# Kernel optimization log

Measured on AMD Instinct MI355X. Metric: run time of the kernel, lower is better.

Reference implementation:

```python
import jax, jax.numpy as jnp
import numpy as np

B, S, H, L, O = 128, 2048, 128, 2, 2  # batch, seq, hidden(=input), layers, output


def setup_inputs() -> dict:
    key = jax.random.key(0)
    k1, k2, k3, k4, k5 = jax.random.split(key, 5)
    std = 1.0 / np.sqrt(H)
    x_data = jax.random.normal(k1, (B, S, H), dtype=jnp.float32)
    x_length = jax.random.randint(k2, (B,), 0, S, dtype=jnp.int32)
    x_label = jax.random.uniform(k3, (B,), dtype=jnp.float32)
    # torch Linear layout: y = x @ W.T ; init uniform(-1/sqrt(H), 1/sqrt(H))
    Wx2h = jax.random.uniform(k4, (L, 2 * H, H), minval=-std, maxval=std, dtype=jnp.float32)
    Wfc = jax.random.uniform(k5, (L, O, H), minval=-std, maxval=std, dtype=jnp.float32)
    return {"x_data": x_data, "x_length": x_length, "x_label": x_label,
            "Wx2h": Wx2h, "Wfc": Wfc}


def reference(x_data, x_length, x_label, Wx2h, Wfc):
    Bn, Sn, Hn = x_data.shape
    Ln = Wx2h.shape[0]
    # valid-timestep mask: seq index < x_length[i]
    mask = (jnp.arange(Sn)[None, :] < x_length[:, None]).astype(x_data.dtype)  # [B,S]

    def step(carry, inp):
        S1, S2 = carry            # each [L,B,H]
        x_t, m_t = inp            # [B,H], [B]
        h = x_t
        out = None
        S1_new, S2_new = [], []
        for l in range(Ln):
            gate = h @ Wx2h[l].T                    # [B,2H]
            m1, m2 = jnp.split(gate, 2, axis=1)
            s1n = S1[l] + jnp.tanh(m1)
            s2n = S2[l] + jnp.tanh(m2)
            Fu = jax.nn.relu(s1n)
            h = (1.0 - Fu) * s2n + Fu * S2[l]       # hy
            out = jax.nn.softmax(h @ Wfc[l].T, axis=1)  # [B,O]
            S1_new.append(s1n)
            S2_new.append(s2n)
        loss_t = m_t * (x_label - jax.nn.sigmoid(out[:, 1])) ** 2  # [B]
        return (jnp.stack(S1_new), jnp.stack(S2_new)), loss_t

    S0 = jnp.zeros((Ln, Bn, Hn), x_data.dtype)
    xs = (jnp.swapaxes(x_data, 0, 1), mask.T)  # time-major [S,B,H], [S,B]
    _, losses = jax.lax.scan(step, (S0, S0), xs)
    return jnp.sum(losses)
```

## Files before the change

### kernel.cpp

```cpp
#include <hip/hip_runtime.h>

typedef __bf16 bf16;
typedef __bf16 bf16x8 __attribute__((ext_vector_type(8)));
typedef float floatx4 __attribute__((ext_vector_type(4)));

#define BATCH 128
#define SEQ   2048
#define HID   128
#define TWOH  256
#define CH    128
#define NCH   16
#define MTOT  (BATCH * SEQ)

__device__ __forceinline__ float fast_tanh(float x) {
    float e = __builtin_amdgcn_exp2f(2.88539008177793f * x);
    return 1.0f - 2.0f * __builtin_amdgcn_rcpf(e + 1.0f);
}
__device__ __forceinline__ float fast_sigmoid(float x) {
    return __builtin_amdgcn_rcpf(1.0f + __builtin_amdgcn_exp2f(-1.44269504088896f * x));
}

union PK4 { unsigned long long u; bf16 h[4]; };

__global__ __launch_bounds__(256) void convert_w_k(const float* __restrict__ W,
                                                   bf16* __restrict__ Wb) {
    int i = blockIdx.x * 256 + threadIdx.x;
    float4 v = ((const float4*)W)[i];
    PK4 pk;
    pk.h[0] = (bf16)v.x; pk.h[1] = (bf16)v.y;
    pk.h[2] = (bf16)v.z; pk.h[3] = (bf16)v.w;
    ((unsigned long long*)Wb)[i] = pk.u;
}

template <int MODE, bool AF32>
__global__ __launch_bounds__(256, 2) void fused_k(const void* __restrict__ Aptr,
                                                  const bf16* __restrict__ Wb,
                                                  const float* __restrict__ Pbase,
                                                  float* __restrict__ Pout,
                                                  bf16* __restrict__ Hb,
                                                  const float* __restrict__ Wfc,
                                                  const int* __restrict__ xlen,
                                                  const float* __restrict__ xlab,
                                                  float* __restrict__ out) {
    __shared__ bf16 As[128 * 128];
    __shared__ bf16 Bs[128 * 128];
    __shared__ float aux[512];
    __shared__ float zbuf[2][128][2];
    __shared__ float red[2];

    const int tid  = threadIdx.x;
    const int lane = tid & 63;
    const int wid  = tid >> 6;
    const int wr   = wid >> 1;
    const int wc   = wid & 1;
    const int quad = lane >> 4;
    const int l16  = lane & 15;
    const long blk = blockIdx.x;
    const long rowBase = blk * 128;

    if (AF32) {
        const float4* A4 = (const float4*)((const float*)Aptr + rowBase * HID);
        #pragma unroll
        for (int it = 0; it < 16; ++it) {
            int i  = it * 256 + tid;
            int r  = i >> 5;
            int c4 = i & 31;
            float4 v = A4[i];
            int g = c4 >> 1, hf = c4 & 1;
            PK4 pk;
            pk.h[0] = (bf16)v.x; pk.h[1] = (bf16)v.y;
            pk.h[2] = (bf16)v.z; pk.h[3] = (bf16)v.w;
            *(unsigned long long*)&As[r * 128 + ((g ^ (r & 7)) << 3) + (hf << 2)] = pk.u;
        }
    } else {
        const uint4* A8 = (const uint4*)((const bf16*)Aptr + rowBase * HID);
        #pragma unroll
        for (int it = 0; it < 8; ++it) {
            int i = it * 256 + tid;
            int r = i >> 4;
            int g = i & 15;
            uint4 v = A8[i];
            *(uint4*)&As[r * 128 + ((g ^ (r & 7)) << 3)] = v;
        }
    }

    float p1[4][4][4];
    float h[4][4][4];

    #pragma unroll
    for (int half = 0; half < 2; ++half) {
        __syncthreads();
        {
            const uint4* W8 = (const uint4*)(Wb + half * 128 * HID);
            #pragma unroll
            for (int it = 0; it < 8; ++it) {
                int i = it * 256 + tid;
                int r = i >> 4;
                int g = i & 15;
                uint4 v = W8[i];
                *(uint4*)&Bs[r * 128 + ((g ^ (r & 7)) << 3)] = v;
            }
        }
        __syncthreads();

        floatx4 acc[4][4];
        #pragma unroll
        for (int a = 0; a < 4; ++a)
            #pragma unroll
            for (int b2 = 0; b2 < 4; ++b2) acc[a][b2] = (floatx4){0.f, 0.f, 0.f, 0.f};

        #pragma unroll
        for (int kk = 0; kk < 128; kk += 32) {
            bf16x8 af[4], bfr[4];
            int kg = (kk >> 3) + quad;
            #pragma unroll
            for (int mi = 0; mi < 4; ++mi) {
                int r = wr * 64 + mi * 16 + l16;
                af[mi] = *(const bf16x8*)&As[r * 128 + ((kg ^ (r & 7)) << 3)];
            }
            #pragma unroll
            for (int ni = 0; ni < 4; ++ni) {
                int n = wc * 64 + ni * 16 + l16;
                bfr[ni] = *(const bf16x8*)&Bs[n * 128 + ((kg ^ (n & 7)) << 3)];
            }
            #pragma unroll
            for (int mi = 0; mi < 4; ++mi)
                #pragma unroll
                for (int ni = 0; ni < 4; ++ni)
                    acc[mi][ni] = __builtin_amdgcn_mfma_f32_16x16x32_bf16(
                        af[mi], bfr[ni], acc[mi][ni], 0, 0, 0);
        }

        float g2loc[4][4][4];
        #pragma unroll
        for (int mi = 0; mi < 4; ++mi)
            #pragma unroll
            for (int ni = 0; ni < 4; ++ni)
                #pragma unroll
                for (int rr = 0; rr < 4; ++rr)
                    g2loc[mi][ni][rr] = fast_tanh(acc[mi][ni][rr]);

        if (MODE == 0) {
            #pragma unroll
            for (int ni = 0; ni < 4; ++ni) {
                float cs = 0.f;
                #pragma unroll
                for (int mi = 0; mi < 4; ++mi)
                    #pragma unroll
                    for (int rr = 0; rr < 4; ++rr) cs += g2loc[mi][ni][rr];
                cs += __shfl_xor(cs, 16);
                cs += __shfl_xor(cs, 32);
                if (quad == 0)
                    aux[wr * 256 + half * 128 + wc * 64 + ni * 16 + l16] = cs;
            }
        } else {
            float pref[4][4][4];
            #pragma unroll
            for (int ni = 0; ni < 4; ++ni) {
                float mibase = 0.f;
                #pragma unroll
                for (int mi = 0; mi < 4; ++mi) {
                    float s0 = g2loc[mi][ni][0];
                    float s1 = s0 + g2loc[mi][ni][1];
                    float s2 = s1 + g2loc[mi][ni][2];
                    float s3 = s2 + g2loc[mi][ni][3];
                    float tot = s3;
                    float xq = tot;
                    float t = __shfl_up(xq, 16);
                    if (quad >= 1) xq += t;
                    t = __shfl_up(xq, 32);
                    if (quad >= 2) xq += t;
                    float excl = mibase + xq - tot;
                    pref[mi][ni][0] = excl + s0;
                    pref[mi][ni][1] = excl + s1;
                    pref[mi][ni][2] = excl + s2;
                    pref[mi][ni][3] = excl + s3;
                    mibase += __shfl(xq, 48 + l16);
                }
                if (wr == 0 && quad == 0)
                    aux[wc * 64 + ni * 16 + l16] = mibase;
            }
            __syncthreads();
            #pragma unroll
            for (int ni = 0; ni < 4; ++ni) {
                int col = half * 128 + wc * 64 + ni * 16 + l16;
                float off = Pbase[(blk << 8) + col];
                if (wr) off += aux[wc * 64 + ni * 16 + l16];
                #pragma unroll
                for (int mi = 0; mi < 4; ++mi)
                    #pragma unroll
                    for (int rr = 0; rr < 4; ++rr)
                        pref[mi][ni][rr] += off;
            }
            if (half == 0) {
                #pragma unroll
                for (int mi = 0; mi < 4; ++mi)
                    #pragma unroll
                    for (int ni = 0; ni < 4; ++ni)
                        #pragma unroll
                        for (int rr = 0; rr < 4; ++rr)
                            p1[mi][ni][rr] = pref[mi][ni][rr];
            } else {
                #pragma unroll
                for (int mi = 0; mi < 4; ++mi)
                    #pragma unroll
                    for (int ni = 0; ni < 4; ++ni)
                        #pragma unroll
                        for (int rr = 0; rr < 4; ++rr)
                            h[mi][ni][rr] = pref[mi][ni][rr] -
                                fmaxf(p1[mi][ni][rr], 0.f) * g2loc[mi][ni][rr];
            }
        }
    }

    if (MODE == 0) {
        __syncthreads();
        Pout[(blk << 8) + tid] = aux[tid] + aux[256 + tid];
    } else if (MODE == 1) {
        #pragma unroll
        for (int mi = 0; mi < 4; ++mi)
            #pragma unroll
            for (int rr = 0; rr < 4; ++rr) {
                long row = rowBase + wr * 64 + mi * 16 + quad * 4 + rr;
                #pragma unroll
                for (int ni = 0; ni < 4; ++ni)
                    Hb[row * HID + wc * 64 + ni * 16 + l16] = (bf16)h[mi][ni][rr];
            }
    } else {
        float w0[4], w1[4];
        #pragma unroll
        for (int ni = 0; ni < 4; ++ni) {
            int c = wc * 64 + ni * 16 + l16;
            w0[ni] = Wfc[2 * HID + c];
            w1[ni] = Wfc[3 * HID + c];
        }
        #pragma unroll
        for (int mi = 0; mi < 4; ++mi)
            #pragma unroll
            for (int rr = 0; rr < 4; ++rr) {
                float z0 = 0.f, z1 = 0.f;
                #pragma unroll
                for (int ni = 0; ni < 4; ++ni) {
                    z0 += h[mi][ni][rr] * w0[ni];
                    z1 += h[mi][ni][rr] * w1[ni];
                }
                z0 += __shfl_xor(z0, 1); z1 += __shfl_xor(z1, 1);
                z0 += __shfl_xor(z0, 2); z1 += __shfl_xor(z1, 2);
                z0 += __shfl_xor(z0, 4); z1 += __shfl_xor(z1, 4);
                z0 += __shfl_xor(z0, 8); z1 += __shfl_xor(z1, 8);
                if (l16 == 0) {
                    int row = wr * 64 + mi * 16 + quad * 4 + rr;
                    zbuf[wc][row][0] = z0;
                    zbuf[wc][row][1] = z1;
                }
            }
        __syncthreads();
        float lsum = 0.f;
        if (tid < 128) {
            int row = tid;
            int b = (int)(blk >> 4), chunk = (int)(blk & 15);
            float z0 = zbuf[0][row][0] + zbuf[1][row][0];
            float z1 = zbuf[0][row][1] + zbuf[1][row][1];
            float o1 = fast_sigmoid(z1 - z0);
            float sg = fast_sigmoid(o1);
            float d = xlab[b] - sg;
            if (chunk * CH + row < xlen[b]) lsum = d * d;
            lsum += __shfl_xor(lsum, 1);
            lsum += __shfl_xor(lsum, 2);
            lsum += __shfl_xor(lsum, 4);
            lsum += __shfl_xor(lsum, 8);
            lsum += __shfl_xor(lsum, 16);
            lsum += __shfl_xor(lsum, 32);
            if (lane == 0) red[tid >> 6] = lsum;
        }
        __syncthreads();
        if (tid == 0) atomicAdd(out, red[0] + red[1]);
    }
}

__global__ __launch_bounds__(256) void scan_partials_k(float* __restrict__ P) {
    int ch = threadIdx.x;
    long b = blockIdx.x;
    float v[NCH];
    #pragma unroll
    for (int c = 0; c < NCH; ++c) v[c] = P[((b * NCH + c) << 8) + ch];
    float run = 0.f;
    #pragma unroll
    for (int c = 0; c < NCH; ++c) {
        float t = v[c];
        P[((b * NCH + c) << 8) + ch] = run;
        run += t;
    }
}

extern "C" void kernel_launch(void* const* d_in, const int* in_sizes, int n_in,
                              void* d_out, int out_size, void* d_ws, size_t ws_size,
                              hipStream_t stream) {
    const float* x    = (const float*)d_in[0];
    const int*   xlen = (const int*)d_in[1];
    const float* xlab = (const float*)d_in[2];
    const float* Wx2h = (const float*)d_in[3];
    const float* Wfc  = (const float*)d_in[4];
    float* out = (float*)d_out;

    char* ws = (char*)d_ws;
    bf16*  Hb = (bf16*)ws;
    float* P  = (float*)(ws + (size_t)MTOT * HID * 2);
    bf16*  Wb = (bf16*)((char*)P + (size_t)BATCH * NCH * TWOH * 4);

    hipMemsetAsync(d_out, 0, sizeof(float), stream);
    convert_w_k<<<64, 256, 0, stream>>>(Wx2h, Wb);

    fused_k<0, true><<<MTOT / 128, 256, 0, stream>>>(x, Wb, nullptr, P, nullptr,
                                                     nullptr, nullptr, nullptr, nullptr);
    scan_partials_k<<<BATCH, 256, 0, stream>>>(P);
    fused_k<1, true><<<MTOT / 128, 256, 0, stream>>>(x, Wb, P, nullptr, Hb,
                                                     nullptr, nullptr, nullptr, nullptr);
    fused_k<0, false><<<MTOT / 128, 256, 0, stream>>>(Hb, Wb + TWOH * HID, nullptr, P,
                                                      nullptr, nullptr, nullptr, nullptr, nullptr);
    scan_partials_k<<<BATCH, 256, 0, stream>>>(P);
    fused_k<2, false><<<MTOT / 128, 256, 0, stream>>>(Hb, Wb + TWOH * HID, P, nullptr,
                                                      nullptr, Wfc, xlen, xlab, out);
}
```

Before: 383.4 us.

## Use 512-thread blocks with 64x32 wave tiles and fuse the epilogue into the second half

Doubles the waves per block from 4 to 8. Each wave now computes a 64x32 tile instead of 64x64, which halves the per-thread accumulator and intermediate register arrays, and the launch bounds now ask for 4 blocks per CU. The h computation, the Hb store and the Wfc projection move into the second-half loop, so the full h array no longer lives in registers. The goal is more resident waves to hide memory latency in these bandwidth-heavy passes, at the cost of more block-level syncs, a 4-way zbuf reduction and smaller MFMA reuse per wave.

```diff
diff --git a/kernel.cpp b/kernel.cpp
--- a/kernel.cpp
+++ b/kernel.cpp
@@ -33,7 +33,7 @@
 }
 
 template <int MODE, bool AF32>
-__global__ __launch_bounds__(256, 2) void fused_k(const void* __restrict__ Aptr,
+__global__ __launch_bounds__(512, 4) void fused_k(const void* __restrict__ Aptr,
                                                   const bf16* __restrict__ Wb,
                                                   const float* __restrict__ Pbase,
                                                   float* __restrict__ Pout,
@@ -45,14 +45,14 @@
     __shared__ bf16 As[128 * 128];
     __shared__ bf16 Bs[128 * 128];
     __shared__ float aux[512];
-    __shared__ float zbuf[2][128][2];
+    __shared__ float zbuf[4][128][2];
     __shared__ float red[2];
 
     const int tid  = threadIdx.x;
     const int lane = tid & 63;
     const int wid  = tid >> 6;
-    const int wr   = wid >> 1;
-    const int wc   = wid & 1;
+    const int wr   = wid >> 2;
+    const int wc   = wid & 3;
     const int quad = lane >> 4;
     const int l16  = lane & 15;
     const long blk = blockIdx.x;
@@ -61,8 +61,8 @@
     if (AF32) {
         const float4* A4 = (const float4*)((const float*)Aptr + rowBase * HID);
         #pragma unroll
-        for (int it = 0; it < 16; ++it) {
-            int i  = it * 256 + tid;
+        for (int it = 0; it < 8; ++it) {
+            int i  = it * 512 + tid;
             int r  = i >> 5;
             int c4 = i & 31;
             float4 v = A4[i];
@@ -75,8 +75,8 @@
     } else {
         const uint4* A8 = (const uint4*)((const bf16*)Aptr + rowBase * HID);
         #pragma unroll
-        for (int it = 0; it < 8; ++it) {
-            int i = it * 256 + tid;
+        for (int it = 0; it < 4; ++it) {
+            int i = it * 512 + tid;
             int r = i >> 4;
             int g = i & 15;
             uint4 v = A8[i];
@@ -84,8 +84,7 @@
         }
     }
 
-    float p1[4][4][4];
-    float h[4][4][4];
+    float p1[4][2][4];
 
     #pragma unroll
     for (int half = 0; half < 2; ++half) {
@@ -93,8 +92,8 @@
         {
             const uint4* W8 = (const uint4*)(Wb + half * 128 * HID);
             #pragma unroll
-            for (int it = 0; it < 8; ++it) {
-                int i = it * 256 + tid;
+            for (int it = 0; it < 4; ++it) {
+                int i = it * 512 + tid;
                 int r = i >> 4;
                 int g = i & 15;
                 uint4 v = W8[i];
@@ -103,15 +102,15 @@
         }
         __syncthreads();
 
-        floatx4 acc[4][4];
+        floatx4 acc[4][2];
         #pragma unroll
         for (int a = 0; a < 4; ++a)
             #pragma unroll
-            for (int b2 = 0; b2 < 4; ++b2) acc[a][b2] = (floatx4){0.f, 0.f, 0.f, 0.f};
+            for (int b2 = 0; b2 < 2; ++b2) acc[a][b2] = (floatx4){0.f, 0.f, 0.f, 0.f};
 
         #pragma unroll
         for (int kk = 0; kk < 128; kk += 32) {
-            bf16x8 af[4], bfr[4];
+            bf16x8 af[4], bfr[2];
             int kg = (kk >> 3) + quad;
             #pragma unroll
             for (int mi = 0; mi < 4; ++mi) {
@@ -119,51 +118,51 @@
                 af[mi] = *(const bf16x8*)&As[r * 128 + ((kg ^ (r & 7)) << 3)];
             }
             #pragma unroll
-            for (int ni = 0; ni < 4; ++ni) {
-                int n = wc * 64 + ni * 16 + l16;
+            for (int ni = 0; ni < 2; ++ni) {
+                int n = wc * 32 + ni * 16 + l16;
                 bfr[ni] = *(const bf16x8*)&Bs[n * 128 + ((kg ^ (n & 7)) << 3)];
             }
             #pragma unroll
             for (int mi = 0; mi < 4; ++mi)
                 #pragma unroll
-                for (int ni = 0; ni < 4; ++ni)
+                for (int ni = 0; ni < 2; ++ni)
                     acc[mi][ni] = __builtin_amdgcn_mfma_f32_16x16x32_bf16(
                         af[mi], bfr[ni], acc[mi][ni], 0, 0, 0);
         }
 
-        float g2loc[4][4][4];
+        float g2[4][2][4];
         #pragma unroll
         for (int mi = 0; mi < 4; ++mi)
             #pragma unroll
-            for (int ni = 0; ni < 4; ++ni)
+            for (int ni = 0; ni < 2; ++ni)
                 #pragma unroll
                 for (int rr = 0; rr < 4; ++rr)
-                    g2loc[mi][ni][rr] = fast_tanh(acc[mi][ni][rr]);
+                    g2[mi][ni][rr] = fast_tanh(acc[mi][ni][rr]);
 
         if (MODE == 0) {
             #pragma unroll
-            for (int ni = 0; ni < 4; ++ni) {
+            for (int ni = 0; ni < 2; ++ni) {
                 float cs = 0.f;
                 #pragma unroll
                 for (int mi = 0; mi < 4; ++mi)
                     #pragma unroll
-                    for (int rr = 0; rr < 4; ++rr) cs += g2loc[mi][ni][rr];
+                    for (int rr = 0; rr < 4; ++rr) cs += g2[mi][ni][rr];
                 cs += __shfl_xor(cs, 16);
                 cs += __shfl_xor(cs, 32);
                 if (quad == 0)
-                    aux[wr * 256 + half * 128 + wc * 64 + ni * 16 + l16] = cs;
+                    aux[wr * 256 + half * 128 + wc * 32 + ni * 16 + l16] = cs;
             }
         } else {
-            float pref[4][4][4];
-            #pragma unroll
-            for (int ni = 0; ni < 4; ++ni) {
+            float pref[4][2][4];
+            #pragma unroll
+            for (int ni = 0; ni < 2; ++ni) {
                 float mibase = 0.f;
                 #pragma unroll
                 for (int mi = 0; mi < 4; ++mi) {
-                    float s0 = g2loc[mi][ni][0];
-                    float s1 = s0 + g2loc[mi][ni][1];
-                    float s2 = s1 + g2loc[mi][ni][2];
-                    float s3 = s2 + g2loc[mi][ni][3];
+                    float s0 = g2[mi][ni][0];
+                    float s1 = s0 + g2[mi][ni][1];
+                    float s2 = s1 + g2[mi][ni][2];
+                    float s3 = s2 + g2[mi][ni][3];
                     float tot = s3;
                     float xq = tot;
                     float t = __shfl_up(xq, 16);
@@ -178,89 +177,87 @@
                     mibase += __shfl(xq, 48 + l16);
                 }
                 if (wr == 0 && quad == 0)
-                    aux[wc * 64 + ni * 16 + l16] = mibase;
+                    aux[wc * 32 + ni * 16 + l16] = mibase;
             }
             __syncthreads();
-            #pragma unroll
-            for (int ni = 0; ni < 4; ++ni) {
-                int col = half * 128 + wc * 64 + ni * 16 + l16;
-                float off = Pbase[(blk << 8) + col];
-                if (wr) off += aux[wc * 64 + ni * 16 + l16];
-                #pragma unroll
-                for (int mi = 0; mi < 4; ++mi)
-                    #pragma unroll
-                    for (int rr = 0; rr < 4; ++rr)
-                        pref[mi][ni][rr] += off;
-            }
+
             if (half == 0) {
                 #pragma unroll
-                for (int mi = 0; mi < 4; ++mi)
-                    #pragma unroll
-                    for (int ni = 0; ni < 4; ++ni)
+                for (int ni = 0; ni < 2; ++ni) {
+                    int col = wc * 32 + ni * 16 + l16;
+                    float off = Pbase[(blk << 8) + col];
+                    if (wr) off += aux[col];
+                    #pragma unroll
+                    for (int mi = 0; mi < 4; ++mi)
                         #pragma unroll
                         for (int rr = 0; rr < 4; ++rr)
-                            p1[mi][ni][rr] = pref[mi][ni][rr];
+                            p1[mi][ni][rr] = pref[mi][ni][rr] + off;
+                }
             } else {
-                #pragma unroll
-                for (int mi = 0; mi < 4; ++mi)
-                    #pragma unroll
-                    for (int ni = 0; ni < 4; ++ni)
+                if (MODE == 1) {
+                    #pragma unroll
+                    for (int ni = 0; ni < 2; ++ni) {
+                        int col = wc * 32 + ni * 16 + l16;
+                        float off = Pbase[(blk << 8) + 128 + col];
+                        if (wr) off += aux[col];
                         #pragma unroll
-                        for (int rr = 0; rr < 4; ++rr)
-                            h[mi][ni][rr] = pref[mi][ni][rr] -
-                                fmaxf(p1[mi][ni][rr], 0.f) * g2loc[mi][ni][rr];
+                        for (int mi = 0; mi < 4; ++mi)
+                            #pragma unroll
+                            for (int rr = 0; rr < 4; ++rr) {
+                                long row = rowBase + wr * 64 + mi * 16 + quad * 4 + rr;
+                                float h = pref[mi][ni][rr] + off -
+                                          fmaxf(p1[mi][ni][rr], 0.f) * g2[mi][ni][rr];
+                                Hb[row * HID + col] = (bf16)h;
+                            }
+                    }
+                } else {
+                    float w0[2], w1[2], off[2];
+                    #pragma unroll
+                    for (int ni = 0; ni < 2; ++ni) {
+                        int col = wc * 32 + ni * 16 + l16;
+                        w0[ni] = Wfc[2 * HID + col];
+                        w1[ni] = Wfc[3 * HID + col];
+                        off[ni] = Pbase[(blk << 8) + 128 + col];
+                        if (wr) off[ni] += aux[col];
+                    }
+                    #pragma unroll
+                    for (int mi = 0; mi < 4; ++mi)
+                        #pragma unroll
+                        for (int rr = 0; rr < 4; ++rr) {
+                            float z0 = 0.f, z1 = 0.f;
+                            #pragma unroll
+                            for (int ni = 0; ni < 2; ++ni) {
+                                float h = pref[mi][ni][rr] + off[ni] -
+                                          fmaxf(p1[mi][ni][rr], 0.f) * g2[mi][ni][rr];
+                                z0 += h * w0[ni];
+                                z1 += h * w1[ni];
+                            }
+                            z0 += __shfl_xor(z0, 1); z1 += __shfl_xor(z1, 1);
+                            z0 += __shfl_xor(z0, 2); z1 += __shfl_xor(z1, 2);
+                            z0 += __shfl_xor(z0, 4); z1 += __shfl_xor(z1, 4);
+                            z0 += __shfl_xor(z0, 8); z1 += __shfl_xor(z1, 8);
+                            if (l16 == 0) {
+                                int row = wr * 64 + mi * 16 + quad * 4 + rr;
+                                zbuf[wc][row][0] = z0;
+                                zbuf[wc][row][1] = z1;
+                            }
+                        }
+                }
             }
         }
     }
 
     if (MODE == 0) {
         __syncthreads();
-        Pout[(blk << 8) + tid] = aux[tid] + aux[256 + tid];
-    } else if (MODE == 1) {
-        #pragma unroll
-        for (int mi = 0; mi < 4; ++mi)
-            #pragma unroll
-            for (int rr = 0; rr < 4; ++rr) {
-                long row = rowBase + wr * 64 + mi * 16 + quad * 4 + rr;
-                #pragma unroll
-                for (int ni = 0; ni < 4; ++ni)
-                    Hb[row * HID + wc * 64 + ni * 16 + l16] = (bf16)h[mi][ni][rr];
-            }
-    } else {
-        float w0[4], w1[4];
-        #pragma unroll
-        for (int ni = 0; ni < 4; ++ni) {
-            int c = wc * 64 + ni * 16 + l16;
-            w0[ni] = Wfc[2 * HID + c];
-            w1[ni] = Wfc[3 * HID + c];
-        }
-        #pragma unroll
-        for (int mi = 0; mi < 4; ++mi)
-            #pragma unroll
-            for (int rr = 0; rr < 4; ++rr) {
-                float z0 = 0.f, z1 = 0.f;
-                #pragma unroll
-                for (int ni = 0; ni < 4; ++ni) {
-                    z0 += h[mi][ni][rr] * w0[ni];
-                    z1 += h[mi][ni][rr] * w1[ni];
-                }
-                z0 += __shfl_xor(z0, 1); z1 += __shfl_xor(z1, 1);
-                z0 += __shfl_xor(z0, 2); z1 += __shfl_xor(z1, 2);
-                z0 += __shfl_xor(z0, 4); z1 += __shfl_xor(z1, 4);
-                z0 += __shfl_xor(z0, 8); z1 += __shfl_xor(z1, 8);
-                if (l16 == 0) {
-                    int row = wr * 64 + mi * 16 + quad * 4 + rr;
-                    zbuf[wc][row][0] = z0;
-                    zbuf[wc][row][1] = z1;
-                }
-            }
+        if (tid < 256) Pout[(blk << 8) + tid] = aux[tid] + aux[256 + tid];
+    } else if (MODE == 2) {
         __syncthreads();
         float lsum = 0.f;
         if (tid < 128) {
             int row = tid;
             int b = (int)(blk >> 4), chunk = (int)(blk & 15);
-            float z0 = zbuf[0][row][0] + zbuf[1][row][0];
-            float z1 = zbuf[0][row][1] + zbuf[1][row][1];
+            float z0 = zbuf[0][row][0] + zbuf[1][row][0] + zbuf[2][row][0] + zbuf[3][row][0];
+            float z1 = zbuf[0][row][1] + zbuf[1][row][1] + zbuf[2][row][1] + zbuf[3][row][1];
             float o1 = fast_sigmoid(z1 - z0);
             float sg = fast_sigmoid(o1);
             float d = xlab[b] - sg;
@@ -271,7 +268,7 @@
             lsum += __shfl_xor(lsum, 8);
             lsum += __shfl_xor(lsum, 16);
             lsum += __shfl_xor(lsum, 32);
-            if (lane == 0) red[tid >> 6] = lsum;
+            if (lane == 0) red[wid] = lsum;
         }
         __syncthreads();
         if (tid == 0) atomicAdd(out, red[0] + red[1]);
@@ -311,14 +308,14 @@
     hipMemsetAsync(d_out, 0, sizeof(float), stream);
     convert_w_k<<<64, 256, 0, stream>>>(Wx2h, Wb);
 
-    fused_k<0, true><<<MTOT / 128, 256, 0, stream>>>(x, Wb, nullptr, P, nullptr,
+    fused_k<0, true><<<MTOT / 128, 512, 0, stream>>>(x, Wb, nullptr, P, nullptr,
                                                      nullptr, nullptr, nullptr, nullptr);
     scan_partials_k<<<BATCH, 256, 0, stream>>>(P);
-    fused_k<1, true><<<MTOT / 128, 256, 0, stream>>>(x, Wb, P, nullptr, Hb,
+    fused_k<1, true><<<MTOT / 128, 512, 0, stream>>>(x, Wb, P, nullptr, Hb,
                                                      nullptr, nullptr, nullptr, nullptr);
-    fused_k<0, false><<<MTOT / 128, 256, 0, stream>>>(Hb, Wb + TWOH * HID, nullptr, P,
+    fused_k<0, false><<<MTOT / 128, 512, 0, stream>>>(Hb, Wb + TWOH * HID, nullptr, P,
                                                       nullptr, nullptr, nullptr, nullptr, nullptr);
     scan_partials_k<<<BATCH, 256, 0, stream>>>(P);
-    fused_k<2, false><<<MTOT / 128, 256, 0, stream>>>(Hb, Wb + TWOH * HID, P, nullptr,
+    fused_k<2, false><<<MTOT / 128, 512, 0, stream>>>(Hb, Wb + TWOH * HID, P, nullptr,
                                                       nullptr, Wfc, xlen, xlab, out);
 }
```

New measurement: 377.0 us. No clear change (-1.7%).
